# Kernel optimization log

Measured on AMD Instinct MI355X. Metric: run time of the kernel, lower is better.

## Reference

```python
import jax, jax.numpy as jnp
import numpy as np
import math

E = 256      # emb_size
H = 4        # num_heads
D = E // H   # head_dim
EXPLORE_SCALE = 0.5
EXPLOIT_SCALE = 0.5
TEMP_MIN = 0.5
TEMP_MAX = 2.0


def setup_inputs() -> dict:
    key = jax.random.key(0)
    ks = jax.random.split(key, 12)
    B, S = 4, 2048
    his_emb = jax.random.normal(ks[0], (B, S, E), dtype=jnp.float32)
    src_key_padding_mask = jax.random.randint(ks[1], (B, S), 0, 2) > 0
    explore = jax.random.uniform(ks[2], (B, S), dtype=jnp.float32)
    exploit = jax.random.uniform(ks[3], (B, S), dtype=jnp.float32)
    scale = 1.0 / math.sqrt(E)
    Wq = jax.random.normal(ks[4], (E, E), dtype=jnp.float32) * scale
    bq = jnp.zeros((E,), dtype=jnp.float32)
    Wk = jax.random.normal(ks[5], (E, E), dtype=jnp.float32) * scale
    bk = jnp.zeros((E,), dtype=jnp.float32)
    Wv = jax.random.normal(ks[6], (E, E), dtype=jnp.float32) * scale
    bv = jnp.zeros((E,), dtype=jnp.float32)
    Wo = jax.random.normal(ks[7], (E, E), dtype=jnp.float32) * scale
    bo = jnp.zeros((E,), dtype=jnp.float32)
    return {"his_emb": his_emb, "src_key_padding_mask": src_key_padding_mask,
            "explore": explore, "exploit": exploit,
            "Wq": Wq, "bq": bq, "Wk": Wk, "bk": bk,
            "Wv": Wv, "bv": bv, "Wo": Wo, "bo": bo}


def reference(his_emb, src_key_padding_mask, explore, exploit,
              Wq, bq, Wk, bk, Wv, bv, Wo, bo):
    B, S, _ = his_emb.shape
    # projections -> [B, H, S, D]
    q = (his_emb @ Wq + bq).reshape(B, S, H, D).transpose(0, 2, 1, 3)
    k = (his_emb @ Wk + bk).reshape(B, S, H, D).transpose(0, 2, 1, 3)
    v = (his_emb @ Wv + bv).reshape(B, S, H, D).transpose(0, 2, 1, 3)
    logits = jnp.einsum('bhqd,bhkd->bhqk', q, k) / math.sqrt(D)
    attn_mask = src_key_padding_mask[:, None, None, :]  # [B,1,1,S] over keys
    logits = jnp.where(attn_mask, -1e16, logits)
    # per-query dynamic temperature
    temp = 1.0 + EXPLORE_SCALE * explore - EXPLOIT_SCALE * exploit  # [B,S]
    temp = jnp.clip(temp, TEMP_MIN, TEMP_MAX)
    temp = jnp.where(src_key_padding_mask, 1.0, temp)
    logits = logits / temp[:, None, :, None]
    probs = jax.nn.softmax(logits, axis=-1)
    probs = jnp.where(attn_mask, 0.0, probs)
    probs = probs / jnp.maximum(probs.sum(axis=-1, keepdims=True), 1e-8)
    out = jnp.einsum('bhqk,bhkd->bhqd', probs, v)
    out = out.transpose(0, 2, 1, 3).reshape(B, S, E)
    out = out @ Wo + bo
    return jnp.where(src_key_padding_mask[:, :, None], 0.0, out)
```

## Files before the change

### kernel.cpp

```cpp
#include <hip/hip_runtime.h>
#include <hip/hip_bf16.h>
#include <math.h>

#define B_ 4
#define S_ 2048
#define E_ 256
#define H_ 4
#define D_ 64
#define NROW (B_*S_)
#define NCH 2
#define CHK (S_/NCH)
#define FM 12.0f

typedef __attribute__((ext_vector_type(8))) short short8;
typedef __attribute__((ext_vector_type(4))) float floatx4;

__device__ __forceinline__ short f2bf(float f){
    union{float f; unsigned u;} x; x.f = f;
    unsigned r = x.u + 0x7fffu + ((x.u>>16)&1u);
    return (short)(r>>16);
}

__global__ __launch_bounds__(256) void transpose_w(
    const float* __restrict__ W0, const float* __restrict__ W1,
    const float* __restrict__ W2, const float* __restrict__ W3,
    short* __restrict__ T0, short* __restrict__ T1,
    short* __restrict__ T2, short* __restrict__ T3)
{
    const float* W = blockIdx.y==0?W0: blockIdx.y==1?W1: blockIdx.y==2?W2:W3;
    short*       T = blockIdx.y==0?T0: blockIdx.y==1?T1: blockIdx.y==2?T2:T3;
    __shared__ float L[64][65];
    const int t = threadIdx.x;
    const int k0 = (blockIdx.x>>2)*64, n0 = (blockIdx.x&3)*64;
    {
        int r = t>>2, c0 = (t&3)*16;
        const float4* p = (const float4*)(W + (size_t)(k0+r)*E_ + n0 + c0);
        #pragma unroll
        for (int j=0;j<4;++j){
            float4 u = p[j];
            L[r][c0+4*j]=u.x; L[r][c0+4*j+1]=u.y; L[r][c0+4*j+2]=u.z; L[r][c0+4*j+3]=u.w;
        }
    }
    __syncthreads();
    {
        int n = t>>2, kk0 = (t&3)*16;
        short8 o0, o1;
        #pragma unroll
        for(int j=0;j<8;++j) o0[j] = f2bf(L[kk0+j][n]);
        #pragma unroll
        for(int j=0;j<8;++j) o1[j] = f2bf(L[kk0+8+j][n]);
        short* dst = T + (size_t)(n0+n)*E_ + k0 + kk0;
        *(short8*)dst = o0; *(short8*)(dst+8) = o1;
    }
}

__global__ __launch_bounds__(256) void qkv_gemm(
    const float* __restrict__ X,
    const short* __restrict__ Wtq, const float* __restrict__ bq,
    const short* __restrict__ Wtk, const float* __restrict__ bk,
    const short* __restrict__ Wtv, const float* __restrict__ bv,
    short* __restrict__ Q, short* __restrict__ K, short* __restrict__ Vt)
{
    const int z = blockIdx.z;
    const short* Wt   = z==0?Wtq: z==1?Wtk:Wtv;
    const float* bias = z==0?bq:  z==1?bk:bv;

    __shared__ __align__(16) short As[64][72];
    __shared__ __align__(16) short Bs[64][72];

    const int t=threadIdx.x, w=t>>6, lane=t&63, ln=lane&15, quad=lane>>4;
    const int m0 = blockIdx.y*64, n0 = blockIdx.x*64;

    floatx4 acc[4] = {};
    for (int kt=0; kt<E_; kt+=64){
        __syncthreads();
        {
            int r=t>>2, c0=(t&3)*16;
            const float4* pa = (const float4*)(X + (size_t)(m0+r)*E_ + kt + c0);
            short8 s0, s1;
            float4 u;
            u=pa[0]; s0[0]=f2bf(u.x); s0[1]=f2bf(u.y); s0[2]=f2bf(u.z); s0[3]=f2bf(u.w);
            u=pa[1]; s0[4]=f2bf(u.x); s0[5]=f2bf(u.y); s0[6]=f2bf(u.z); s0[7]=f2bf(u.w);
            u=pa[2]; s1[0]=f2bf(u.x); s1[1]=f2bf(u.y); s1[2]=f2bf(u.z); s1[3]=f2bf(u.w);
            u=pa[3]; s1[4]=f2bf(u.x); s1[5]=f2bf(u.y); s1[6]=f2bf(u.z); s1[7]=f2bf(u.w);
            *(short8*)&As[r][c0] = s0; *(short8*)&As[r][c0+8] = s1;
            const uint4* pb = (const uint4*)(Wt + (size_t)(n0+r)*E_ + kt + c0);
            *(uint4*)&Bs[r][c0] = pb[0]; *(uint4*)&Bs[r][c0+8] = pb[1];
        }
        __syncthreads();
        short8 a0 = *(const short8*)&As[w*16+ln][quad*8];
        short8 a1 = *(const short8*)&As[w*16+ln][32+quad*8];
        #pragma unroll
        for (int c=0;c<4;++c){
            short8 b0 = *(const short8*)&Bs[c*16+ln][quad*8];
            short8 b1 = *(const short8*)&Bs[c*16+ln][32+quad*8];
            acc[c] = __builtin_amdgcn_mfma_f32_16x16x32_bf16(a0,b0,acc[c],0,0,0);
            acc[c] = __builtin_amdgcn_mfma_f32_16x16x32_bf16(a1,b1,acc[c],0,0,0);
        }
    }
    if (z<2){
        short* dst = z==0?Q:K;
        #pragma unroll
        for(int c=0;c<4;++c){
            int colg = n0 + c*16 + ln;
            float bia = bias[colg];
            #pragma unroll
            for(int reg=0;reg<4;++reg){
                int row = m0 + w*16 + quad*4 + reg;
                dst[(size_t)row*E_ + colg] = f2bf(acc[c][reg] + bia);
            }
        }
    } else {
        #pragma unroll
        for(int c=0;c<4;++c){
            int colg = n0 + c*16 + ln;
            int hx = colg>>6, d = colg&63;
            float bia = bias[colg];
            #pragma unroll
            for(int reg=0;reg<4;++reg){
                int row = m0 + w*16 + quad*4 + reg;
                int bb = row>>11, s = row&(S_-1);
                Vt[((size_t)((bb*H_+hx)*D_+d))*S_ + s] = f2bf(acc[c][reg] + bia);
            }
        }
    }
}

__global__ __launch_bounds__(256) void attn_mfma(
    const short* __restrict__ Qb, const short* __restrict__ Kb, const short* __restrict__ Vtb,
    const int* __restrict__ mask,
    const float* __restrict__ explore, const float* __restrict__ exploit,
    float* __restrict__ OP, float* __restrict__ Lb)
{
    const int z = blockIdx.z;
    const int b = z>>2, h = z&3;
    const int q0 = blockIdx.x*64;
    const int ck = blockIdx.y;
    const int k0 = ck*CHK;
    const int t=threadIdx.x, w=t>>6, lane=t&63, ln=lane&15, quad=lane>>4;

    __shared__ __align__(16) short Ks[64][72];
    __shared__ __align__(16) short Vs[64][72];
    __shared__ __align__(16) short Ps[4][16][72];
    __shared__ float mb[64];

    float tsc[4], lacc[4];
    #pragma unroll
    for (int reg=0; reg<4; ++reg){
        int qg = q0 + w*16 + quad*4 + reg;
        float ex = explore[b*S_+qg], xp = exploit[b*S_+qg];
        float tmp = fminf(fmaxf(1.0f + 0.5f*ex - 0.5f*xp, 0.5f), 2.0f);
        if (mask[b*S_+qg]) tmp = 1.0f;
        tsc[reg]  = 1.0f/(tmp*8.0f);
        lacc[reg] = 0.0f;
    }
    const size_t qrow = (size_t)(b*S_ + q0 + w*16 + ln)*E_ + h*D_;
    short8 qa0 = *(const short8*)(Qb + qrow + quad*8);
    short8 qa1 = *(const short8*)(Qb + qrow + 32 + quad*8);

    floatx4 of[4] = {};

    for (int kt=k0; kt<k0+CHK; kt+=64){
        __syncthreads();
        {
            int r=t>>2, c0=(t&3)*16;
            const uint4* gk = (const uint4*)(Kb + (size_t)(b*S_+kt+r)*E_ + h*D_ + c0);
            *(uint4*)&Ks[r][c0] = gk[0]; *(uint4*)&Ks[r][c0+8] = gk[1];
            const uint4* gv = (const uint4*)(Vtb + ((size_t)((b*H_+h)*D_+r))*S_ + kt + c0);
            *(uint4*)&Vs[r][c0] = gv[0]; *(uint4*)&Vs[r][c0+8] = gv[1];
        }
        if (t<64) mb[t] = mask[b*S_+kt+t] ? -1e30f : 0.0f;
        __syncthreads();

        floatx4 sf[4];
        #pragma unroll
        for (int c=0;c<4;++c){
            short8 kb0 = *(const short8*)&Ks[c*16+ln][quad*8];
            short8 kb1 = *(const short8*)&Ks[c*16+ln][32+quad*8];
            floatx4 zz = {};
            zz = __builtin_amdgcn_mfma_f32_16x16x32_bf16(qa0,kb0,zz,0,0,0);
            zz = __builtin_amdgcn_mfma_f32_16x16x32_bf16(qa1,kb1,zz,0,0,0);
            sf[c] = zz;
        }

        float mbc[4];
        #pragma unroll
        for(int c=0;c<4;++c) mbc[c] = mb[c*16+ln];

        #pragma unroll
        for(int reg=0;reg<4;++reg){
            #pragma unroll
            for(int c=0;c<4;++c){
                float p = __expf(sf[c][reg]*tsc[reg] + mbc[c] - FM);
                Ps[w][quad*4+reg][c*16+ln] = f2bf(p);
                lacc[reg] += p;
            }
        }

        short8 pa0 = *(const short8*)&Ps[w][ln][quad*8];
        short8 pa1 = *(const short8*)&Ps[w][ln][32+quad*8];
        #pragma unroll
        for(int dc=0;dc<4;++dc){
            short8 vb0 = *(const short8*)&Vs[dc*16+ln][quad*8];
            short8 vb1 = *(const short8*)&Vs[dc*16+ln][32+quad*8];
            of[dc] = __builtin_amdgcn_mfma_f32_16x16x32_bf16(pa0,vb0,of[dc],0,0,0);
            of[dc] = __builtin_amdgcn_mfma_f32_16x16x32_bf16(pa1,vb1,of[dc],0,0,0);
        }
    }

    #pragma unroll
    for(int reg=0;reg<4;++reg){
        float l = lacc[reg];
        l += __shfl_xor(l,1); l += __shfl_xor(l,2);
        l += __shfl_xor(l,4); l += __shfl_xor(l,8);
        int qg = q0 + w*16 + quad*4 + reg;
        float* dst = OP + (((size_t)(ck*B_+b)*H_+h)*S_ + qg)*D_;
        #pragma unroll
        for(int dc=0;dc<4;++dc) dst[dc*16+ln] = of[dc][reg];
        if (ln==0) Lb[((size_t)(ck*B_+b)*H_+h)*S_ + qg] = l;
    }
}

__global__ __launch_bounds__(256) void combine(
    const float* __restrict__ OP, const float* __restrict__ Lb, short* __restrict__ CTXb)
{
    int gid = blockIdx.x*256 + threadIdx.x;
    #pragma unroll
    for (int i=0;i<4;++i){
        int idx = gid + i*524288;
        int e = idx & 255, row = idx >> 8;
        int bb = row >> 11, s = row & (S_-1);
        int hh = e >> 6, d = e & 63;
        float o = 0.f, l = 0.f;
        #pragma unroll
        for (int c=0;c<NCH;++c){
            o += OP[(((size_t)(c*B_+bb)*H_+hh)*S_+s)*D_ + d];
            l += Lb[((size_t)(c*B_+bb)*H_+hh)*S_+s];
        }
        CTXb[idx] = f2bf(o / fmaxf(l, 1e-8f));
    }
}

__global__ __launch_bounds__(256) void out_gemm(
    const short* __restrict__ Ab, const short* __restrict__ Wto, const float* __restrict__ bo,
    const int* __restrict__ mask, float* __restrict__ out)
{
    __shared__ __align__(16) short As[64][72];
    __shared__ __align__(16) short Bs[64][72];
    const int t=threadIdx.x, w=t>>6, lane=t&63, ln=lane&15, quad=lane>>4;
    const int m0 = blockIdx.y*64, n0 = blockIdx.x*64;
    floatx4 acc[4] = {};
    for (int kt=0; kt<E_; kt+=64){
        __syncthreads();
        {
            int r=t>>2, c0=(t&3)*16;
            const uint4* pa = (const uint4*)(Ab + (size_t)(m0+r)*E_ + kt + c0);
            *(uint4*)&As[r][c0] = pa[0]; *(uint4*)&As[r][c0+8] = pa[1];
            const uint4* pb = (const uint4*)(Wto + (size_t)(n0+r)*E_ + kt + c0);
            *(uint4*)&Bs[r][c0] = pb[0]; *(uint4*)&Bs[r][c0+8] = pb[1];
        }
        __syncthreads();
        short8 a0 = *(const short8*)&As[w*16+ln][quad*8];
        short8 a1 = *(const short8*)&As[w*16+ln][32+quad*8];
        #pragma unroll
        for (int c=0;c<4;++c){
            short8 b0 = *(const short8*)&Bs[c*16+ln][quad*8];
            short8 b1 = *(const short8*)&Bs[c*16+ln][32+quad*8];
            acc[c] = __builtin_amdgcn_mfma_f32_16x16x32_bf16(a0,b0,acc[c],0,0,0);
            acc[c] = __builtin_amdgcn_mfma_f32_16x16x32_bf16(a1,b1,acc[c],0,0,0);
        }
    }
    #pragma unroll
    for(int c=0;c<4;++c){
        int colg = n0 + c*16 + ln;
        float bia = bo[colg];
        #pragma unroll
        for(int reg=0;reg<4;++reg){
            int row = m0 + w*16 + quad*4 + reg;
            out[(size_t)row*E_ + colg] = mask[row] ? 0.0f : (acc[c][reg] + bia);
        }
    }
}

extern "C" void kernel_launch(void* const* d_in, const int* in_sizes, int n_in,
                              void* d_out, int out_size, void* d_ws, size_t ws_size,
                              hipStream_t stream) {
    const float* his     = (const float*)d_in[0];
    const int*   mask    = (const int*)d_in[1];
    const float* explore = (const float*)d_in[2];
    const float* exploit = (const float*)d_in[3];
    const float* Wq = (const float*)d_in[4];
    const float* bq = (const float*)d_in[5];
    const float* Wk = (const float*)d_in[6];
    const float* bk = (const float*)d_in[7];
    const float* Wv = (const float*)d_in[8];
    const float* bv = (const float*)d_in[9];
    const float* Wo = (const float*)d_in[10];
    const float* bo = (const float*)d_in[11];

    char* ws = (char*)d_ws;
    const size_t NE2 = (size_t)NROW * E_ * 2;
    short* Wtq  = (short*)(ws);                    ws += E_*E_*2;
    short* Wtk  = (short*)(ws);                    ws += E_*E_*2;
    short* Wtv  = (short*)(ws);                    ws += E_*E_*2;
    short* Wto  = (short*)(ws);                    ws += E_*E_*2;
    short* Qb   = (short*)(ws);                    ws += NE2;
    short* Kb   = (short*)(ws);                    ws += NE2;
    short* Vtb  = (short*)(ws);                    ws += NE2;
    float* OP   = (float*)(ws);                    ws += (size_t)NCH*NROW*E_*4;
    float* Lb   = (float*)(ws);                    ws += (size_t)NCH*B_*H_*S_*4;
    short* CTXb = Qb;

    transpose_w<<<dim3(16,4), 256, 0, stream>>>(Wq, Wk, Wv, Wo, Wtq, Wtk, Wtv, Wto);

    qkv_gemm<<<dim3(E_/64, NROW/64, 3), 256, 0, stream>>>(
        his, Wtq, bq, Wtk, bk, Wtv, bv, Qb, Kb, Vtb);

    attn_mfma<<<dim3(S_/64, NCH, B_*H_), 256, 0, stream>>>(
        Qb, Kb, Vtb, mask, explore, exploit, OP, Lb);

    combine<<<2048, 256, 0, stream>>>(OP, Lb, CTXb);

    out_gemm<<<dim3(E_/64, NROW/64), 256, 0, stream>>>(CTXb, Wto, bo, mask, (float*)d_out);
}
```

Before: 146.3 us.

## Restructure attention tiling, prescale Q, bf16 partials, pre-convert X

Converts the input activations to bf16 once in a separate kernel, and folds the per-query temperature and 1/sqrt(D) scaling into the Q projection epilogue. The attention kernel now handles 128 queries per block (32 per wave), stores K in an XOR-swizzled LDS tile, and reads V directly from global memory instead of staging it in LDS. It truncates P to bf16 with a byte permute and writes bf16 partial outputs. The key dimension is split into 4 chunks instead of 2, and the combine step reads bf16 partials. The goal is to cut conversion work, LDS traffic and partial-output bandwidth, and to raise parallelism. The cost is an extra launch, plus some precision loss from truncating P and rounding Q and the partials to bf16.

```diff
diff --git a/kernel.cpp b/kernel.cpp
--- a/kernel.cpp
+++ b/kernel.cpp
@@ -8,7 +8,7 @@
 #define H_ 4
 #define D_ 64
 #define NROW (B_*S_)
-#define NCH 2
+#define NCH 4
 #define CHK (S_/NCH)
 #define FM 12.0f
 
@@ -19,6 +19,22 @@
     union{float f; unsigned u;} x; x.f = f;
     unsigned r = x.u + 0x7fffu + ((x.u>>16)&1u);
     return (short)(r>>16);
+}
+__device__ __forceinline__ float bf2f(short s){
+    union{unsigned u; float f;} x; x.u = ((unsigned)(unsigned short)s)<<16; return x.f;
+}
+__device__ __forceinline__ unsigned pk_trunc(float lo, float hi){
+    return __builtin_amdgcn_perm(__float_as_uint(hi), __float_as_uint(lo), 0x07060302u);
+}
+
+__global__ __launch_bounds__(256) void convert_x(const float* __restrict__ X, short* __restrict__ Xb){
+    int gid = blockIdx.x*256 + threadIdx.x;
+    const float4* p = (const float4*)(X + (size_t)gid*8);
+    float4 a = p[0], b = p[1];
+    short8 o;
+    o[0]=f2bf(a.x); o[1]=f2bf(a.y); o[2]=f2bf(a.z); o[3]=f2bf(a.w);
+    o[4]=f2bf(b.x); o[5]=f2bf(b.y); o[6]=f2bf(b.z); o[7]=f2bf(b.w);
+    *(short8*)(Xb + (size_t)gid*8) = o;
 }
 
 __global__ __launch_bounds__(256) void transpose_w(
@@ -55,10 +71,12 @@
 }
 
 __global__ __launch_bounds__(256) void qkv_gemm(
-    const float* __restrict__ X,
+    const short* __restrict__ Xb,
     const short* __restrict__ Wtq, const float* __restrict__ bq,
     const short* __restrict__ Wtk, const float* __restrict__ bk,
     const short* __restrict__ Wtv, const float* __restrict__ bv,
+    const int* __restrict__ mask,
+    const float* __restrict__ explore, const float* __restrict__ exploit,
     short* __restrict__ Q, short* __restrict__ K, short* __restrict__ Vt)
 {
     const int z = blockIdx.z;
@@ -76,14 +94,8 @@
         __syncthreads();
         {
             int r=t>>2, c0=(t&3)*16;
-            const float4* pa = (const float4*)(X + (size_t)(m0+r)*E_ + kt + c0);
-            short8 s0, s1;
-            float4 u;
-            u=pa[0]; s0[0]=f2bf(u.x); s0[1]=f2bf(u.y); s0[2]=f2bf(u.z); s0[3]=f2bf(u.w);
-            u=pa[1]; s0[4]=f2bf(u.x); s0[5]=f2bf(u.y); s0[6]=f2bf(u.z); s0[7]=f2bf(u.w);
-            u=pa[2]; s1[0]=f2bf(u.x); s1[1]=f2bf(u.y); s1[2]=f2bf(u.z); s1[3]=f2bf(u.w);
-            u=pa[3]; s1[4]=f2bf(u.x); s1[5]=f2bf(u.y); s1[6]=f2bf(u.z); s1[7]=f2bf(u.w);
-            *(short8*)&As[r][c0] = s0; *(short8*)&As[r][c0+8] = s1;
+            const uint4* pa = (const uint4*)(Xb + (size_t)(m0+r)*E_ + kt + c0);
+            *(uint4*)&As[r][c0] = pa[0]; *(uint4*)&As[r][c0+8] = pa[1];
             const uint4* pb = (const uint4*)(Wt + (size_t)(n0+r)*E_ + kt + c0);
             *(uint4*)&Bs[r][c0] = pb[0]; *(uint4*)&Bs[r][c0+8] = pb[1];
         }
@@ -98,8 +110,15 @@
             acc[c] = __builtin_amdgcn_mfma_f32_16x16x32_bf16(a1,b1,acc[c],0,0,0);
         }
     }
-    if (z<2){
-        short* dst = z==0?Q:K;
+    if (z==0){
+        float tscr[4];
+        #pragma unroll
+        for(int reg=0;reg<4;++reg){
+            int row = m0 + w*16 + quad*4 + reg;
+            float ex = explore[row], xp = exploit[row];
+            float tmp = fminf(fmaxf(1.0f + 0.5f*ex - 0.5f*xp, 0.5f), 2.0f);
+            tscr[reg] = mask[row] ? 0.125f : 1.0f/(8.0f*tmp);
+        }
         #pragma unroll
         for(int c=0;c<4;++c){
             int colg = n0 + c*16 + ln;
@@ -107,7 +126,18 @@
             #pragma unroll
             for(int reg=0;reg<4;++reg){
                 int row = m0 + w*16 + quad*4 + reg;
-                dst[(size_t)row*E_ + colg] = f2bf(acc[c][reg] + bia);
+                Q[(size_t)row*E_ + colg] = f2bf((acc[c][reg] + bia)*tscr[reg]);
+            }
+        }
+    } else if (z==1){
+        #pragma unroll
+        for(int c=0;c<4;++c){
+            int colg = n0 + c*16 + ln;
+            float bia = bias[colg];
+            #pragma unroll
+            for(int reg=0;reg<4;++reg){
+                int row = m0 + w*16 + quad*4 + reg;
+                K[(size_t)row*E_ + colg] = f2bf(acc[c][reg] + bia);
             }
         }
     } else {
@@ -126,103 +156,100 @@
     }
 }
 
-__global__ __launch_bounds__(256) void attn_mfma(
+__global__ __launch_bounds__(256,4) void attn_mfma(
     const short* __restrict__ Qb, const short* __restrict__ Kb, const short* __restrict__ Vtb,
     const int* __restrict__ mask,
-    const float* __restrict__ explore, const float* __restrict__ exploit,
-    float* __restrict__ OP, float* __restrict__ Lb)
-{
-    const int z = blockIdx.z;
-    const int b = z>>2, h = z&3;
-    const int q0 = blockIdx.x*64;
-    const int ck = blockIdx.y;
-    const int k0 = ck*CHK;
+    short* __restrict__ OP, float* __restrict__ Lb)
+{
+    const int bh = blockIdx.z;
+    const int b = bh>>2, h = bh&3;
+    const int q0 = blockIdx.x*128;
+    const int ck = blockIdx.y, k0 = ck*CHK;
     const int t=threadIdx.x, w=t>>6, lane=t&63, ln=lane&15, quad=lane>>4;
 
-    __shared__ __align__(16) short Ks[64][72];
-    __shared__ __align__(16) short Vs[64][72];
-    __shared__ __align__(16) short Ps[4][16][72];
-    __shared__ float mb[64];
-
-    float tsc[4], lacc[4];
+    __shared__ __align__(16) short Ks[64*64];
+    __shared__ __align__(16) short Ps[4][32][72];
+    __shared__ float mv[64];
+
+    short8 qa[2][2];
     #pragma unroll
-    for (int reg=0; reg<4; ++reg){
-        int qg = q0 + w*16 + quad*4 + reg;
-        float ex = explore[b*S_+qg], xp = exploit[b*S_+qg];
-        float tmp = fminf(fmaxf(1.0f + 0.5f*ex - 0.5f*xp, 0.5f), 2.0f);
-        if (mask[b*S_+qg]) tmp = 1.0f;
-        tsc[reg]  = 1.0f/(tmp*8.0f);
-        lacc[reg] = 0.0f;
-    }
-    const size_t qrow = (size_t)(b*S_ + q0 + w*16 + ln)*E_ + h*D_;
-    short8 qa0 = *(const short8*)(Qb + qrow + quad*8);
-    short8 qa1 = *(const short8*)(Qb + qrow + 32 + quad*8);
-
-    floatx4 of[4] = {};
+    for (int qh=0; qh<2; ++qh){
+        const short* qr = Qb + (size_t)(b*S_ + q0 + w*32 + qh*16 + ln)*E_ + h*D_;
+        qa[qh][0] = *(const short8*)(qr + quad*8);
+        qa[qh][1] = *(const short8*)(qr + 32 + quad*8);
+    }
+
+    const int sr = t>>2, scc = (t&3)*2;
+    short* kst0 = &Ks[sr*64 + ((scc  )^(sr&7))*8];
+    short* kst1 = &Ks[sr*64 + ((scc+1)^(sr&7))*8];
+    const short* kgl = Kb + (size_t)(b*S_ + sr)*E_ + h*D_ + scc*8;
+
+    floatx4 of[2][4] = {};
+    float lacc[2] = {0.f, 0.f};
 
     for (int kt=k0; kt<k0+CHK; kt+=64){
         __syncthreads();
         {
-            int r=t>>2, c0=(t&3)*16;
-            const uint4* gk = (const uint4*)(Kb + (size_t)(b*S_+kt+r)*E_ + h*D_ + c0);
-            *(uint4*)&Ks[r][c0] = gk[0]; *(uint4*)&Ks[r][c0+8] = gk[1];
-            const uint4* gv = (const uint4*)(Vtb + ((size_t)((b*H_+h)*D_+r))*S_ + kt + c0);
-            *(uint4*)&Vs[r][c0] = gv[0]; *(uint4*)&Vs[r][c0+8] = gv[1];
-        }
-        if (t<64) mb[t] = mask[b*S_+kt+t] ? -1e30f : 0.0f;
-        __syncthreads();
-
-        floatx4 sf[4];
+            const uint4* g = (const uint4*)(kgl + (size_t)kt*E_);
+            *(uint4*)kst0 = g[0];
+            *(uint4*)kst1 = g[1];
+        }
+        if (t<64) mv[t] = (mask[b*S_+kt+t] ? -1e30f : 0.0f) - FM;
+        __syncthreads();
+
         #pragma unroll
         for (int c=0;c<4;++c){
-            short8 kb0 = *(const short8*)&Ks[c*16+ln][quad*8];
-            short8 kb1 = *(const short8*)&Ks[c*16+ln][32+quad*8];
-            floatx4 zz = {};
-            zz = __builtin_amdgcn_mfma_f32_16x16x32_bf16(qa0,kb0,zz,0,0,0);
-            zz = __builtin_amdgcn_mfma_f32_16x16x32_bf16(qa1,kb1,zz,0,0,0);
-            sf[c] = zz;
-        }
-
-        float mbc[4];
-        #pragma unroll
-        for(int c=0;c<4;++c) mbc[c] = mb[c*16+ln];
-
-        #pragma unroll
-        for(int reg=0;reg<4;++reg){
-            #pragma unroll
-            for(int c=0;c<4;++c){
-                float p = __expf(sf[c][reg]*tsc[reg] + mbc[c] - FM);
-                Ps[w][quad*4+reg][c*16+ln] = f2bf(p);
-                lacc[reg] += p;
-            }
-        }
-
-        short8 pa0 = *(const short8*)&Ps[w][ln][quad*8];
-        short8 pa1 = *(const short8*)&Ps[w][ln][32+quad*8];
-        #pragma unroll
-        for(int dc=0;dc<4;++dc){
-            short8 vb0 = *(const short8*)&Vs[dc*16+ln][quad*8];
-            short8 vb1 = *(const short8*)&Vs[dc*16+ln][32+quad*8];
-            of[dc] = __builtin_amdgcn_mfma_f32_16x16x32_bf16(pa0,vb0,of[dc],0,0,0);
-            of[dc] = __builtin_amdgcn_mfma_f32_16x16x32_bf16(pa1,vb1,of[dc],0,0,0);
+            short8 ka0 = *(const short8*)&Ks[(c*16+ln)*64 + ((quad  )^(ln&7))*8];
+            short8 ka1 = *(const short8*)&Ks[(c*16+ln)*64 + ((4+quad)^(ln&7))*8];
+            float4 mvv = *(const float4*)&mv[c*16+quad*4];
+            #pragma unroll
+            for (int qh=0; qh<2; ++qh){
+                floatx4 s = {};
+                s = __builtin_amdgcn_mfma_f32_16x16x32_bf16(ka0, qa[qh][0], s, 0,0,0);
+                s = __builtin_amdgcn_mfma_f32_16x16x32_bf16(ka1, qa[qh][1], s, 0,0,0);
+                float p0 = __expf(s[0] + mvv.x);
+                float p1 = __expf(s[1] + mvv.y);
+                float p2 = __expf(s[2] + mvv.z);
+                float p3 = __expf(s[3] + mvv.w);
+                lacc[qh] += (p0+p1)+(p2+p3);
+                uint2 pw; pw.x = pk_trunc(p0,p1); pw.y = pk_trunc(p2,p3);
+                *(uint2*)&Ps[w][qh*16+ln][c*16+quad*4] = pw;
+            }
+        }
+
+        #pragma unroll
+        for (int half=0; half<2; ++half){
+            short8 pa0 = *(const short8*)&Ps[w][ln]   [half*32 + quad*8];
+            short8 pa1 = *(const short8*)&Ps[w][16+ln][half*32 + quad*8];
+            #pragma unroll
+            for (int dc=0; dc<4; ++dc){
+                short8 vb = *(const short8*)(Vtb + ((size_t)(bh*D_ + dc*16+ln))*S_ + kt + half*32 + quad*8);
+                of[0][dc] = __builtin_amdgcn_mfma_f32_16x16x32_bf16(pa0, vb, of[0][dc], 0,0,0);
+                of[1][dc] = __builtin_amdgcn_mfma_f32_16x16x32_bf16(pa1, vb, of[1][dc], 0,0,0);
+            }
         }
     }
 
     #pragma unroll
-    for(int reg=0;reg<4;++reg){
-        float l = lacc[reg];
-        l += __shfl_xor(l,1); l += __shfl_xor(l,2);
-        l += __shfl_xor(l,4); l += __shfl_xor(l,8);
-        int qg = q0 + w*16 + quad*4 + reg;
-        float* dst = OP + (((size_t)(ck*B_+b)*H_+h)*S_ + qg)*D_;
-        #pragma unroll
-        for(int dc=0;dc<4;++dc) dst[dc*16+ln] = of[dc][reg];
-        if (ln==0) Lb[((size_t)(ck*B_+b)*H_+h)*S_ + qg] = l;
+    for (int qh=0; qh<2; ++qh){
+        float l = lacc[qh];
+        l += __shfl_xor(l, 16);
+        l += __shfl_xor(l, 32);
+        #pragma unroll
+        for (int dc=0; dc<4; ++dc){
+            #pragma unroll
+            for (int reg=0; reg<4; ++reg){
+                int q = q0 + w*32 + qh*16 + quad*4 + reg;
+                OP[((size_t)(ck*16 + bh)*S_ + q)*D_ + dc*16 + ln] = f2bf(of[qh][dc][reg]);
+            }
+        }
+        if (quad==0)
+            Lb[(size_t)(ck*16 + bh)*S_ + q0 + w*32 + qh*16 + ln] = l;
     }
 }
 
 __global__ __launch_bounds__(256) void combine(
-    const float* __restrict__ OP, const float* __restrict__ Lb, short* __restrict__ CTXb)
+    const short* __restrict__ OP, const float* __restrict__ Lb, short* __restrict__ CTXb)
 {
     int gid = blockIdx.x*256 + threadIdx.x;
     #pragma unroll
@@ -231,11 +258,12 @@
         int e = idx & 255, row = idx >> 8;
         int bb = row >> 11, s = row & (S_-1);
         int hh = e >> 6, d = e & 63;
+        int bh = bb*H_ + hh;
         float o = 0.f, l = 0.f;
         #pragma unroll
         for (int c=0;c<NCH;++c){
-            o += OP[(((size_t)(c*B_+bb)*H_+hh)*S_+s)*D_ + d];
-            l += Lb[((size_t)(c*B_+bb)*H_+hh)*S_+s];
+            o += bf2f(OP[((size_t)(c*16 + bh)*S_ + s)*D_ + d]);
+            l += Lb[(size_t)(c*16 + bh)*S_ + s];
         }
         CTXb[idx] = f2bf(o / fmaxf(l, 1e-8f));
     }
@@ -307,17 +335,19 @@
     short* Qb   = (short*)(ws);                    ws += NE2;
     short* Kb   = (short*)(ws);                    ws += NE2;
     short* Vtb  = (short*)(ws);                    ws += NE2;
-    float* OP   = (float*)(ws);                    ws += (size_t)NCH*NROW*E_*4;
+    short* OP   = (short*)(ws);                    ws += (size_t)NCH*B_*H_*S_*D_*2;
     float* Lb   = (float*)(ws);                    ws += (size_t)NCH*B_*H_*S_*4;
+    short* Xb   = OP;
     short* CTXb = Qb;
 
+    convert_x<<<1024, 256, 0, stream>>>(his, Xb);
     transpose_w<<<dim3(16,4), 256, 0, stream>>>(Wq, Wk, Wv, Wo, Wtq, Wtk, Wtv, Wto);
 
     qkv_gemm<<<dim3(E_/64, NROW/64, 3), 256, 0, stream>>>(
-        his, Wtq, bq, Wtk, bk, Wtv, bv, Qb, Kb, Vtb);
-
-    attn_mfma<<<dim3(S_/64, NCH, B_*H_), 256, 0, stream>>>(
-        Qb, Kb, Vtb, mask, explore, exploit, OP, Lb);
+        Xb, Wtq, bq, Wtk, bk, Wtv, bv, mask, explore, exploit, Qb, Kb, Vtb);
+
+    attn_mfma<<<dim3(S_/128, NCH, B_*H_), 256, 0, stream>>>(
+        Qb, Kb, Vtb, mask, OP, Lb);
 
     combine<<<2048, 256, 0, stream>>>(OP, Lb, CTXb);
 
```

Measured after the change: 152.1 us. 4.0% more time.
